# Kernel tuning notes

Hardware: AMD Instinct MI355X
Metric: run time of the kernel (lower is better)

Reference implementation:

```python
import jax, jax.numpy as jnp
import numpy as np

H = 4    # heads
DK = 5   # d_k = d_model // h = 20 // 4
D = 20   # d_model


def _proj(x, W, b):
    # x: [B,S,D] -> [B,H,S,DK]
    B, S, _ = x.shape
    y = x @ W.T + b
    return y.reshape(B, S, H, DK).transpose(0, 2, 1, 3)


def _attn(q, k, v, mask4):
    # q,k,v: [B,H,S,DK]; mask4: [B,1,1,S]
    scores = jnp.einsum('bhqd,bhkd->bhqk', q, k) / jnp.sqrt(jnp.asarray(DK, q.dtype))
    scores = jnp.where(mask4 == 0, jnp.asarray(-1e9, q.dtype), scores)
    p = jax.nn.softmax(scores, axis=-1)  # dropout omitted (eval mode)
    return jnp.einsum('bhqk,bhkd->bhqd', p, v)


def setup_inputs() -> dict:
    key = jax.random.key(0)
    ks = jax.random.split(key, 12)
    B, S = 8, 2048
    scale = 1.0 / np.sqrt(D)
    inp = {
        'query': jax.random.normal(ks[0], (B, S, D), dtype=jnp.float32),
        'key': jax.random.normal(ks[1], (B, S, D), dtype=jnp.float32),
        'value': jax.random.normal(ks[2], (B, S, D), dtype=jnp.float32),
        'mask': jax.random.randint(ks[3], (B, S), 0, 2, dtype=jnp.int32),
    }
    for i in range(4):
        inp[f'W{i}'] = jax.random.normal(ks[4 + 2 * i], (D, D), dtype=jnp.float32) * scale
        inp[f'b{i}'] = jax.random.normal(ks[5 + 2 * i], (D,), dtype=jnp.float32) * 0.01
    return inp


def reference(query, key, value, mask, W0, b0, W1, b1, W2, b2, W3, b3):
    B, S, _ = query.shape
    mask4 = mask[:, None, None, :]  # [B,1,1,S]
    # Six permuted (arg-to-linear0, arg-to-linear1, arg-to-linear2) variants,
    # exactly as the torch forward: (q,k,k),(k,q,q),(q,v,v),(v,q,q),(k,v,v),(v,k,k)
    triples = [
        (query, key, key), (key, query, query),
        (query, value, value), (value, query, query),
        (key, value, value), (value, key, key),
    ]
    out = None
    for a, bb, c in triples:
        o = _attn(_proj(a, W0, b0), _proj(bb, W1, b1), _proj(c, W2, b2), mask4)
        out = o if out is None else out + o
    # merge heads: [B,H,S,DK] -> [B,S,D]
    out = out.transpose(0, 2, 1, 3).reshape(B, S, H * DK)
    return out @ W3.T + b3
```

## Files before the change

### kernel.cpp

```cpp
#include <hip/hip_runtime.h>
#include <cstdint>
#include <cstddef>

#define B    8
#define SEQ  2048
#define H    4
#define DKN  5
#define DIM  20
#define PRE8 8
#define SENTB ((short)0xC2FC)
#define ONEB  ((short)0x3F80)
#define B128  ((short)0x4300)
#define PBIASM 12599162.0f

typedef short short8 __attribute__((ext_vector_type(8)));
typedef float f32x16 __attribute__((ext_vector_type(16)));

static __device__ __forceinline__ unsigned short bf16b(float x) {
    union { float f; unsigned u; } v; v.f = x;
    unsigned r = v.u + 0x7FFFu + ((v.u >> 16) & 1u);
    return (unsigned short)(r >> 16);
}
static __device__ __forceinline__ float bf16f(unsigned short h) {
    union { unsigned u; float f; } v; v.u = ((unsigned)h) << 16;
    return v.f;
}
static __device__ __forceinline__ unsigned pk_pbits(float ta, float tb) {
    unsigned ia, ib;
    __builtin_memcpy(&ia, &ta, 4);
    __builtin_memcpy(&ib, &tb, 4);
    return __builtin_amdgcn_perm(ib, ia, 0x05040100u);
}
static __device__ __forceinline__ int sig32(int t) {
    return (t & 19) | ((t & 4) << 1) | ((t & 8) >> 1);
}


__global__ __launch_bounds__(256) void proj_kernel(
    const float* __restrict__ q, const float* __restrict__ k, const float* __restrict__ v,
    const float* __restrict__ W0, const float* __restrict__ b0,
    const float* __restrict__ W1, const float* __restrict__ b1,
    const float* __restrict__ W2, const float* __restrict__ b2,
    const int* __restrict__ mask,
    short* __restrict__ Qt, short* __restrict__ Kt, short* __restrict__ Vt,
    int* __restrict__ meta)
{
    __shared__ float Ws[3][DIM * DIM];
    __shared__ float bsh[3][DIM];
    __shared__ int   widx[256];
    __shared__ int   cntS;

    int tid = threadIdx.x;
    int blk = blockIdx.x;
    int w   = blk & 7;  blk >>= 3;
    int h   = blk & 3;  blk >>= 2;
    int bb  = blk & 7;  blk >>= 3;
    int x   = blk;
    int s0  = w * 256;

    for (int i = tid; i < DIM * DIM; i += 256) {
        Ws[0][i] = W0[i]; Ws[1][i] = W1[i]; Ws[2][i] = W2[i];
    }
    if (tid < DIM) { bsh[0][tid] = b0[tid]; bsh[1][tid] = b1[tid]; bsh[2][tid] = b2[tid]; }

    if (tid < 64) {
        const int* mrow = mask + bb * SEQ;
        int base = 0;
        for (int ch = 0; ch < SEQ; ch += 64) {
            int mv = mrow[ch + tid];
            unsigned long long bal = __ballot(mv != 0);
            int pos = base + (int)__popcll(bal & ((1ull << tid) - 1ull));
            if (mv && pos >= s0 && pos < s0 + 256) widx[pos - s0] = ch + tid;
            base += (int)__popcll(bal);
        }
        if (tid == 0) {
            cntS = base;
            if (x == 0 && h == 0 && w == 0) meta[bb] = base;
        }
    }
    __syncthreads();

    int  cnt   = cntS;
    int  c     = s0 + tid;
    bool valid = c < cnt;
    int  gs    = valid ? widx[tid] : 0;

    const float QSC = 0.44721359549995793f * 1.4426950408889634f * 128.0f;
    const float* base = (x == 0) ? q : ((x == 1) ? k : v);

    float xq[DIM], xg[DIM];
    {
        const float4* r4 = (const float4*)(base + (size_t)(bb * SEQ + c) * DIM);
        const float4* g4 = (const float4*)(base + (size_t)(bb * SEQ + gs) * DIM);
        #pragma unroll
        for (int i = 0; i < 5; ++i) {
            float4 a = r4[i], g = g4[i];
            xq[i*4+0]=a.x; xq[i*4+1]=a.y; xq[i*4+2]=a.z; xq[i*4+3]=a.w;
            xg[i*4+0]=g.x; xg[i*4+1]=g.y; xg[i*4+2]=g.z; xg[i*4+3]=g.w;
        }
    }

    #define DOT20(xv, t, j, dst) {                                        \
        float acc_ = bsh[t][j];                                           \
        const float4* wr_ = (const float4*)&Ws[t][(j) * DIM];             \
        _Pragma("unroll")                                                 \
        for (int i4 = 0; i4 < 5; ++i4) {                                  \
            float4 w_ = wr_[i4];                                          \
            acc_ += (xv)[i4*4+0]*w_.x + (xv)[i4*4+1]*w_.y                 \
                  + (xv)[i4*4+2]*w_.z + (xv)[i4*4+3]*w_.w;                \
        }                                                                 \
        dst = acc_;                                                       \
    }

    size_t row = ((size_t)(x * B + bb) * H + h) * SEQ + c;

    short8 qhi = {0, 0, 0, 0, 0, B128, 0, 0};
    short8 qlo = {0, 0, 0, 0, 0, 0, 0, 0};
    #pragma unroll
    for (int d = 0; d < DKN; ++d) {
        float y; DOT20(xq, 0, h * DKN + d, y);
        y *= QSC;
        unsigned short hb = bf16b(y);
        qhi[d] = (short)hb;
        qlo[d] = (short)bf16b(y - bf16f(hb));
    }
    ((short8*)Qt)[row * 2 + 0] = qhi;
    ((short8*)Qt)[row * 2 + 1] = qlo;

    short8 rk = {0, 0, 0, 0, 0, valid ? (short)0 : SENTB, 0, 0};
    if (valid) {
        #pragma unroll
        for (int d = 0; d < DKN; ++d) {
            float y; DOT20(xg, 1, h * DKN + d, y);
            rk[d] = (short)bf16b(y);
        }
    }
    ((short8*)Kt)[row] = rk;

    if (valid) {
        size_t vb = ((size_t)(x * B + bb) * H + h) * 8 * SEQ;
        int vcol = (c & ~31) + sig32(c & 31);
        #pragma unroll
        for (int d = 0; d < DKN; ++d) {
            float y; DOT20(xg, 2, h * DKN + d, y);
            Vt[vb + (size_t)d * SEQ + vcol] = (short)bf16b(y);
        }
        Vt[vb + (size_t)5 * SEQ + vcol] = ONEB;
    }
}

__global__ __launch_bounds__(128) void attn_kernel(
    const short* __restrict__ Qt, const short* __restrict__ Kt,
    const short* __restrict__ Vt, const int* __restrict__ meta,
    float* __restrict__ pre)
{
    int lane = threadIdx.x & 63;
    int l31  = lane & 31, half = lane >> 5;

    int wid  = blockIdx.x;
    int qtp  = wid / 192;
    int grp  = wid - qtp * 192;
    int qt   = qtp * 2 + (threadIdx.x >> 6);
    int h    = grp & 3;  grp >>= 2;
    int b    = grp & 7;  grp >>= 3;
    int p    = grp;
    int a    = (0x212010 >> (4 * p)) & 0xF;
    int kv   = (0x120201 >> (4 * p)) & 0xF;

    int cnt  = meta[b];
    int kend = (cnt + 63) & ~63;

    const short*  Qb = Qt + ((size_t)(a  * B + b) * H + h) * SEQ * 16;
    const short8* Kb = (const short8*)Kt + ((size_t)(kv * B + b) * H + h) * SEQ;
    const short*  Vb = Vt + ((size_t)(kv * B + b) * H + h) * 8 * SEQ;
    const short*  Vr = Vb + (size_t)(l31 & 7) * SEQ + half * 8;

    short8 qf[4];
    f32x16 acc[4];
    f32x16 zc = {0.f,0.f,0.f,0.f,0.f,0.f,0.f,0.f,0.f,0.f,0.f,0.f,0.f,0.f,0.f,0.f};
    f32x16 sb = {PBIASM,PBIASM,PBIASM,PBIASM,PBIASM,PBIASM,PBIASM,PBIASM,
                 PBIASM,PBIASM,PBIASM,PBIASM,PBIASM,PBIASM,PBIASM,PBIASM};
    #pragma unroll
    for (int t = 0; t < 4; ++t) {
        int qb = qt * 32 + t * 512;
        qf[t]  = *(const short8*)(Qb + (size_t)(qb + l31) * 16 + half * 8);
        acc[t] = zc;
    }

    short8 kfA = Kb[l31],      kfB = Kb[32 + l31];
    short8 vaA = *(const short8*)(Vr);
    short8 vcA = *(const short8*)(Vr + 16);
    short8 vaB = *(const short8*)(Vr + 32);
    short8 vcB = *(const short8*)(Vr + 48);

    for (int c0 = 0; c0 < kend; c0 += 64) {
        int c1 = c0 + 64;
        short8 kfA_n = Kb[c1 + l31];
        short8 kfB_n = Kb[c1 + 32 + l31];
        short8 vaA_n = *(const short8*)(Vr + c1);
        short8 vcA_n = *(const short8*)(Vr + c1 + 16);
        short8 vaB_n = *(const short8*)(Vr + c1 + 32);
        short8 vcB_n = *(const short8*)(Vr + c1 + 48);

        #pragma unroll
        for (int t = 0; t < 4; ++t) {
            f32x16 dA = __builtin_amdgcn_mfma_f32_32x32x16_bf16(kfA, qf[t], sb, 0, 0, 0);
            unsigned p0[4], p1[4];
            #pragma unroll
            for (int r = 0; r < 4; ++r) {
                p0[r] = pk_pbits(dA[2 * r],     dA[2 * r + 1]);
                p1[r] = pk_pbits(dA[2 * r + 8], dA[2 * r + 9]);
            }
            short8 f0, f1;
            __builtin_memcpy(&f0, p0, 16);
            __builtin_memcpy(&f1, p1, 16);
            acc[t] = __builtin_amdgcn_mfma_f32_32x32x16_bf16(vaA, f0, acc[t], 0, 0, 0);
            acc[t] = __builtin_amdgcn_mfma_f32_32x32x16_bf16(vcA, f1, acc[t], 0, 0, 0);

            f32x16 dB = __builtin_amdgcn_mfma_f32_32x32x16_bf16(kfB, qf[t], sb, 0, 0, 0);
            #pragma unroll
            for (int r = 0; r < 4; ++r) {
                p0[r] = pk_pbits(dB[2 * r],     dB[2 * r + 1]);
                p1[r] = pk_pbits(dB[2 * r + 8], dB[2 * r + 9]);
            }
            __builtin_memcpy(&f0, p0, 16);
            __builtin_memcpy(&f1, p1, 16);
            acc[t] = __builtin_amdgcn_mfma_f32_32x32x16_bf16(vaB, f0, acc[t], 0, 0, 0);
            acc[t] = __builtin_amdgcn_mfma_f32_32x32x16_bf16(vcB, f1, acc[t], 0, 0, 0);
        }

        kfA = kfA_n; kfB = kfB_n;
        vaA = vaA_n; vcA = vcA_n; vaB = vaB_n; vcB = vcB_n;
    }

    float* base0 = pre + (((size_t)p * B + b) * H + h) * SEQ * PRE8;
    #pragma unroll
    for (int t = 0; t < 4; ++t) {
        int qb = qt * 32 + t * 512;
        float lv  = __shfl(acc[t][1], 32 + l31, 64);
        float inv = 1.0f / lv;
        float* dst = base0 + (size_t)(qb + l31) * PRE8;
        if (half == 0)
            *(float4*)dst = make_float4(acc[t][0]*inv, acc[t][1]*inv,
                                        acc[t][2]*inv, acc[t][3]*inv);
        else
            dst[4] = acc[t][0] * inv;
    }
}

__global__ __launch_bounds__(256) void final_kernel(
    const float* __restrict__ pre,
    const float* __restrict__ W3, const float* __restrict__ b3,
    float* __restrict__ out)
{
    __shared__ float Ws[DIM * DIM];
    __shared__ float bs[DIM];
    int tid = threadIdx.x;
    for (int i = tid; i < DIM * DIM; i += 256) Ws[i] = W3[i];
    if (tid < DIM) bs[tid] = b3[tid];
    __syncthreads();

    int g = blockIdx.x * 256 + tid;
    int b = g / SEQ;
    int s = g - b * SEQ;

    float x[DIM];
    #pragma unroll
    for (int i = 0; i < DIM; ++i) x[i] = 0.f;

    for (int p = 0; p < 6; ++p) {
        #pragma unroll
        for (int h = 0; h < H; ++h) {
            const float* sr = pre + (((size_t)p * B + b) * H + h) * SEQ * PRE8
                                  + (size_t)s * PRE8;
            float4 a = *(const float4*)sr;
            float  a4 = sr[4];
            x[h * DKN + 0] += a.x; x[h * DKN + 1] += a.y; x[h * DKN + 2] += a.z;
            x[h * DKN + 3] += a.w; x[h * DKN + 4] += a4;
        }
    }

    float y[DIM];
    for (int j = 0; j < DIM; ++j) {
        float acc = bs[j];
        const float4* wr = (const float4*)&Ws[j * DIM];
        #pragma unroll
        for (int i4 = 0; i4 < 5; ++i4) {
            float4 w = wr[i4];
            acc += x[i4*4+0]*w.x + x[i4*4+1]*w.y + x[i4*4+2]*w.z + x[i4*4+3]*w.w;
        }
        y[j] = acc;
    }
    float4* dst = (float4*)(out + (size_t)(b * SEQ + s) * DIM);
    #pragma unroll
    for (int j4 = 0; j4 < 5; ++j4)
        dst[j4] = make_float4(y[j4*4+0], y[j4*4+1], y[j4*4+2], y[j4*4+3]);
}

extern "C" void kernel_launch(void* const* d_in, const int* in_sizes, int n_in,
                              void* d_out, int out_size, void* d_ws, size_t ws_size,
                              hipStream_t stream) {
    const float* q    = (const float*)d_in[0];
    const float* k    = (const float*)d_in[1];
    const float* v    = (const float*)d_in[2];
    const int*   mask = (const int*)d_in[3];
    const float* W0 = (const float*)d_in[4];  const float* b0 = (const float*)d_in[5];
    const float* W1 = (const float*)d_in[6];  const float* b1 = (const float*)d_in[7];
    const float* W2 = (const float*)d_in[8];  const float* b2 = (const float*)d_in[9];
    const float* W3 = (const float*)d_in[10]; const float* b3 = (const float*)d_in[11];

    const size_t NROW = (size_t)3 * B * H * SEQ;
    short* Qt = (short*)d_ws;
    short* Kt = Qt + NROW * 16;
    short* Vt = Kt + NROW * 8;
    float* pre = (float*)(Vt + NROW * 8);
    int*   meta = (int*)(pre + (size_t)6 * B * H * SEQ * PRE8);
    float* out = (float*)d_out;

    proj_kernel<<<dim3(3 * B * H * (SEQ / 256)), dim3(256), 0, stream>>>(
        q, k, v, W0, b0, W1, b1, W2, b2, mask, Qt, Kt, Vt, meta);
    attn_kernel<<<dim3(6 * B * H * 16 / 2), dim3(128), 0, stream>>>(
        Qt, Kt, Vt, meta, pre);
    final_kernel<<<dim3(B * SEQ / 256), dim3(256), 0, stream>>>(pre, W3, b3, out);
}
```

Baseline: 149.8 us.

## Re-tile V layout into 32-key blocks, halve per-wave query tiles, raise priority

Reorganizes the V workspace so each 32-key chunk of all 8 dk rows is contiguous, which makes per-iteration V loads local. The attention kernel now gives each wave 2 query tiles instead of 4 and launches twice as many blocks, with a launch-bounds occupancy hint. The loop is split into A/B halves with the next loads issued in between and s_setprio around the MFMA sections. The final kernel uses 64-thread blocks to spread work over more CUs. The aim is more parallelism and better latency hiding, at the cost of reloading K/V more often per query tile.

Measured after the change: 144.0 us. 1.04x faster.

```diff
diff --git a/kernel.cpp b/kernel.cpp
--- a/kernel.cpp
+++ b/kernel.cpp
@@ -139,17 +139,17 @@
 
     if (valid) {
         size_t vb = ((size_t)(x * B + bb) * H + h) * 8 * SEQ;
-        int vcol = (c & ~31) + sig32(c & 31);
+        size_t vcell = vb + (size_t)(c >> 5) * 256 + sig32(c & 31);
         #pragma unroll
         for (int d = 0; d < DKN; ++d) {
             float y; DOT20(xg, 2, h * DKN + d, y);
-            Vt[vb + (size_t)d * SEQ + vcol] = (short)bf16b(y);
-        }
-        Vt[vb + (size_t)5 * SEQ + vcol] = ONEB;
-    }
-}
-
-__global__ __launch_bounds__(128) void attn_kernel(
+            Vt[vcell + (size_t)d * 32] = (short)bf16b(y);
+        }
+        Vt[vcell + (size_t)5 * 32] = ONEB;
+    }
+}
+
+__global__ __launch_bounds__(128, 4) void attn_kernel(
     const short* __restrict__ Qt, const short* __restrict__ Kt,
     const short* __restrict__ Vt, const int* __restrict__ meta,
     float* __restrict__ pre)
@@ -158,14 +158,14 @@
     int l31  = lane & 31, half = lane >> 5;
 
     int wid  = blockIdx.x;
-    int qtp  = wid / 192;
-    int grp  = wid - qtp * 192;
-    int qt   = qtp * 2 + (threadIdx.x >> 6);
+    int qtq  = wid / 192;
+    int grp  = wid - qtq * 192;
     int h    = grp & 3;  grp >>= 2;
     int b    = grp & 7;  grp >>= 3;
     int p    = grp;
     int a    = (0x212010 >> (4 * p)) & 0xF;
     int kv   = (0x120201 >> (4 * p)) & 0xF;
+    int qt0  = qtq * 4 + (threadIdx.x >> 6) * 2;
 
     int cnt  = meta[b];
     int kend = (cnt + 63) & ~63;
@@ -173,16 +173,16 @@
     const short*  Qb = Qt + ((size_t)(a  * B + b) * H + h) * SEQ * 16;
     const short8* Kb = (const short8*)Kt + ((size_t)(kv * B + b) * H + h) * SEQ;
     const short*  Vb = Vt + ((size_t)(kv * B + b) * H + h) * 8 * SEQ;
-    const short*  Vr = Vb + (size_t)(l31 & 7) * SEQ + half * 8;
-
-    short8 qf[4];
-    f32x16 acc[4];
+    const short*  Vr = Vb + (size_t)(l31 & 7) * 32 + half * 8;
+
+    short8 qf[2];
+    f32x16 acc[2];
     f32x16 zc = {0.f,0.f,0.f,0.f,0.f,0.f,0.f,0.f,0.f,0.f,0.f,0.f,0.f,0.f,0.f,0.f};
     f32x16 sb = {PBIASM,PBIASM,PBIASM,PBIASM,PBIASM,PBIASM,PBIASM,PBIASM,
                  PBIASM,PBIASM,PBIASM,PBIASM,PBIASM,PBIASM,PBIASM,PBIASM};
     #pragma unroll
-    for (int t = 0; t < 4; ++t) {
-        int qb = qt * 32 + t * 512;
+    for (int t = 0; t < 2; ++t) {
+        int qb = (qt0 + t) * 32;
         qf[t]  = *(const short8*)(Qb + (size_t)(qb + l31) * 16 + half * 8);
         acc[t] = zc;
     }
@@ -190,20 +190,20 @@
     short8 kfA = Kb[l31],      kfB = Kb[32 + l31];
     short8 vaA = *(const short8*)(Vr);
     short8 vcA = *(const short8*)(Vr + 16);
-    short8 vaB = *(const short8*)(Vr + 32);
-    short8 vcB = *(const short8*)(Vr + 48);
+    short8 vaB = *(const short8*)(Vr + 256);
+    short8 vcB = *(const short8*)(Vr + 272);
 
     for (int c0 = 0; c0 < kend; c0 += 64) {
         int c1 = c0 + 64;
+        const short* Vn = Vr + (size_t)c1 * 8;
+
         short8 kfA_n = Kb[c1 + l31];
-        short8 kfB_n = Kb[c1 + 32 + l31];
-        short8 vaA_n = *(const short8*)(Vr + c1);
-        short8 vcA_n = *(const short8*)(Vr + c1 + 16);
-        short8 vaB_n = *(const short8*)(Vr + c1 + 32);
-        short8 vcB_n = *(const short8*)(Vr + c1 + 48);
-
-        #pragma unroll
-        for (int t = 0; t < 4; ++t) {
+        short8 vaA_n = *(const short8*)(Vn);
+        short8 vcA_n = *(const short8*)(Vn + 16);
+
+        __builtin_amdgcn_s_setprio(1);
+        #pragma unroll
+        for (int t = 0; t < 2; ++t) {
             f32x16 dA = __builtin_amdgcn_mfma_f32_32x32x16_bf16(kfA, qf[t], sb, 0, 0, 0);
             unsigned p0[4], p1[4];
             #pragma unroll
@@ -216,27 +216,38 @@
             __builtin_memcpy(&f1, p1, 16);
             acc[t] = __builtin_amdgcn_mfma_f32_32x32x16_bf16(vaA, f0, acc[t], 0, 0, 0);
             acc[t] = __builtin_amdgcn_mfma_f32_32x32x16_bf16(vcA, f1, acc[t], 0, 0, 0);
-
+        }
+        __builtin_amdgcn_s_setprio(0);
+        kfA = kfA_n; vaA = vaA_n; vcA = vcA_n;
+
+        short8 kfB_n = Kb[c1 + 32 + l31];
+        short8 vaB_n = *(const short8*)(Vn + 256);
+        short8 vcB_n = *(const short8*)(Vn + 272);
+
+        __builtin_amdgcn_s_setprio(1);
+        #pragma unroll
+        for (int t = 0; t < 2; ++t) {
             f32x16 dB = __builtin_amdgcn_mfma_f32_32x32x16_bf16(kfB, qf[t], sb, 0, 0, 0);
+            unsigned p0[4], p1[4];
             #pragma unroll
             for (int r = 0; r < 4; ++r) {
                 p0[r] = pk_pbits(dB[2 * r],     dB[2 * r + 1]);
                 p1[r] = pk_pbits(dB[2 * r + 8], dB[2 * r + 9]);
             }
+            short8 f0, f1;
             __builtin_memcpy(&f0, p0, 16);
             __builtin_memcpy(&f1, p1, 16);
             acc[t] = __builtin_amdgcn_mfma_f32_32x32x16_bf16(vaB, f0, acc[t], 0, 0, 0);
             acc[t] = __builtin_amdgcn_mfma_f32_32x32x16_bf16(vcB, f1, acc[t], 0, 0, 0);
         }
-
-        kfA = kfA_n; kfB = kfB_n;
-        vaA = vaA_n; vcA = vcA_n; vaB = vaB_n; vcB = vcB_n;
+        __builtin_amdgcn_s_setprio(0);
+        kfB = kfB_n; vaB = vaB_n; vcB = vcB_n;
     }
 
     float* base0 = pre + (((size_t)p * B + b) * H + h) * SEQ * PRE8;
     #pragma unroll
-    for (int t = 0; t < 4; ++t) {
-        int qb = qt * 32 + t * 512;
+    for (int t = 0; t < 2; ++t) {
+        int qb = (qt0 + t) * 32;
         float lv  = __shfl(acc[t][1], 32 + l31, 64);
         float inv = 1.0f / lv;
         float* dst = base0 + (size_t)(qb + l31) * PRE8;
@@ -248,7 +259,7 @@
     }
 }
 
-__global__ __launch_bounds__(256) void final_kernel(
+__global__ __launch_bounds__(64) void final_kernel(
     const float* __restrict__ pre,
     const float* __restrict__ W3, const float* __restrict__ b3,
     float* __restrict__ out)
@@ -256,11 +267,11 @@
     __shared__ float Ws[DIM * DIM];
     __shared__ float bs[DIM];
     int tid = threadIdx.x;
-    for (int i = tid; i < DIM * DIM; i += 256) Ws[i] = W3[i];
+    for (int i = tid; i < DIM * DIM; i += 64) Ws[i] = W3[i];
     if (tid < DIM) bs[tid] = b3[tid];
     __syncthreads();
 
-    int g = blockIdx.x * 256 + tid;
+    int g = blockIdx.x * 64 + tid;
     int b = g / SEQ;
     int s = g - b * SEQ;
 
@@ -319,7 +330,7 @@
 
     proj_kernel<<<dim3(3 * B * H * (SEQ / 256)), dim3(256), 0, stream>>>(
         q, k, v, W0, b0, W1, b1, W2, b2, mask, Qt, Kt, Vt, meta);
-    attn_kernel<<<dim3(6 * B * H * 16 / 2), dim3(128), 0, stream>>>(
+    attn_kernel<<<dim3(6 * B * H * 16), dim3(128), 0, stream>>>(
         Qt, Kt, Vt, meta, pre);
-    final_kernel<<<dim3(B * SEQ / 256), dim3(256), 0, stream>>>(pre, W3, b3, out);
-}
+    final_kernel<<<dim3(B * SEQ / 64), dim3(64), 0, stream>>>(pre, W3, b3, out);
+}
```
